# Kernel tuning notes

Hardware: AMD Instinct MI355X
Metric: run time of the kernel (lower is better)

Reference implementation:

```python
import jax, jax.numpy as jnp
import numpy as np
import math

NUM_HEADS = 16
ATTN_WIDTH = 256


def setup_inputs() -> dict:
    key = jax.random.key(0)
    ks = jax.random.split(key, 5)
    B, S, C, H = 2, 2048, 1024, 1024
    scale = 0.02
    return {
        "x": jax.random.normal(ks[0], (B, S, C), dtype=jnp.float32),
        "Wq": jax.random.normal(ks[1], (C, H), dtype=jnp.float32) * scale,
        "Wk": jax.random.normal(ks[2], (C, H), dtype=jnp.float32) * scale,
        "Wv": jax.random.normal(ks[3], (C, H), dtype=jnp.float32) * scale,
        "Wo": jax.random.normal(ks[4], (H, C), dtype=jnp.float32) * scale,
    }


def reference(x, Wq, Wk, Wv, Wo):
    B, S, C = x.shape
    H = NUM_HEADS
    dh = Wq.shape[1] // H  # head dim; Q.size(-1) in torch code

    def split_heads(t):
        # [B, S, H*dh] -> [B, H, S, dh]
        return t.reshape(B, S, H, dh).transpose(0, 2, 1, 3)

    q = split_heads(x @ Wq)
    k = split_heads(x @ Wk)
    v = split_heads(x @ Wv)

    scores = jnp.einsum("bhqd,bhkd->bhqk", q, k) / math.sqrt(dh)
    # exp-shift (first 'softmax-like' step, unnormalized)
    scores = jnp.exp(scores - jnp.max(scores, axis=-1, keepdims=True))
    # banded mask: tril(attn_width//2 - 1).triu(-(attn_width//2))
    i = jnp.arange(S)[:, None]
    j = jnp.arange(S)[None, :]
    d = j - i
    half = ATTN_WIDTH // 2
    mask = (d <= half - 1) & (d >= -half)
    scores = jnp.where(mask, scores, 0.0)
    # second softmax over the masked exp-scores (zeros contribute exp(0)=1)
    weights = jax.nn.softmax(scores, axis=-1)

    out = jnp.einsum("bhqk,bhkd->bhqd", weights, v)  # [B, H, S, dh]
    out = out.transpose(0, 2, 1, 3).reshape(B, S, H * dh)
    return out @ Wo
```

## Files before the change

kernel.cpp:

```cpp
#include <hip/hip_runtime.h>
#include <math.h>

typedef __bf16 bf16_t;
typedef bf16_t bf16x8 __attribute__((ext_vector_type(8)));
typedef bf16_t bf16x4 __attribute__((ext_vector_type(4)));
typedef float f32x4 __attribute__((ext_vector_type(4)));

constexpr int S_ = 2048;
constexpr float SCALE = 0.125f;

#define MFMA_B16(a, b, c) __builtin_amdgcn_mfma_f32_16x16x32_bf16(a, b, c, 0, 0, 0)

#define WAIT_VM0() __builtin_amdgcn_s_waitcnt(0x0F70)
#define WAIT_VM4() __builtin_amdgcn_s_waitcnt(0x0F74)
#define BARRIER()  __builtin_amdgcn_s_barrier()

typedef __attribute__((address_space(1))) const void* as1_cvp;
typedef __attribute__((address_space(3))) void* as3_vp;

__device__ __forceinline__ void gl2lds16(const void* g, void* l)
{
    __builtin_amdgcn_global_load_lds((as1_cvp)g, (as3_vp)l, 16, 0, 0);
}

#define SRC_SWZ8(lane) ((((lane) & 3) ^ (((lane) >> 3) & 3)) * 8)
#define RD_SWZ8(quad, l15) ((((quad) ^ (((l15) >> 1) & 3))) * 8)

__global__ __launch_bounds__(256) void prep(const float* __restrict__ x,
                                            const float* __restrict__ Wq,
                                            const float* __restrict__ Wk,
                                            const float* __restrict__ Wv,
                                            const float* __restrict__ Wo,
                                            bf16_t* __restrict__ xb,
                                            bf16_t* __restrict__ Wqt,
                                            bf16_t* __restrict__ Wkt,
                                            bf16_t* __restrict__ Wvt,
                                            bf16_t* __restrict__ Wot,
                                            float* __restrict__ vsp)
{
    __shared__ float T[64][65];
    const int blk = blockIdx.x;
    const int tid = threadIdx.x;
    if (blk < 1024) {
#pragma unroll
        for (int u = 0; u < 4; ++u) {
            const int g = blk * 1024 + u * 256 + tid;
            const float4 v = ((const float4*)x)[g];
            bf16x4 o;
            o[0] = (bf16_t)v.x; o[1] = (bf16_t)v.y;
            o[2] = (bf16_t)v.z; o[3] = (bf16_t)v.w;
            *(bf16x4*)&xb[(size_t)g * 4] = o;
        }
    } else if (blk < 2048) {
        const int rem = blk - 1024;
        const int wsel = rem >> 8, t = rem & 255;
        const float* src = (wsel == 0) ? Wq : (wsel == 1) ? Wk : (wsel == 2) ? Wv : Wo;
        bf16_t* dst = (wsel == 0) ? Wqt : (wsel == 1) ? Wkt : (wsel == 2) ? Wvt : Wot;
        const int k0 = (t >> 4) * 64, n0 = (t & 15) * 64;
        const int rr = tid >> 4, c4 = (tid & 15) * 4;
#pragma unroll
        for (int u = 0; u < 4; ++u) {
            const float4 v = *(const float4*)&src[(size_t)(k0 + u * 16 + rr) * 1024 + n0 + c4];
            T[u * 16 + rr][c4 + 0] = v.x; T[u * 16 + rr][c4 + 1] = v.y;
            T[u * 16 + rr][c4 + 2] = v.z; T[u * 16 + rr][c4 + 3] = v.w;
        }
        __syncthreads();
#pragma unroll
        for (int u = 0; u < 4; ++u) {
            bf16x4 o;
#pragma unroll
            for (int e = 0; e < 4; ++e) o[e] = (bf16_t)T[c4 + e][u * 16 + rr];
            *(bf16x4*)&dst[(size_t)(n0 + u * 16 + rr) * 1024 + k0 + c4] = o;
        }
    } else {
#pragma unroll
        for (int u = 0; u < 8; ++u) vsp[u * 256 + tid] = 0.f;
    }
}

template <int MODE>
__device__ __forceinline__ void mfma_gemm_body(const bf16_t* __restrict__ A,
                                               const bf16_t* __restrict__ Bt,
                                               void* __restrict__ dst,
                                               float* __restrict__ vsum_out,
                                               int m0, int n0)
{
    __shared__ bf16_t As[12288];
    __shared__ bf16_t Bs[12288];

    const int tid = threadIdx.x;
    const int lane = tid & 63, wid = tid >> 6;
    const int l15 = lane & 15, quad = lane >> 4;
    const int wm = (wid & 1) * 64, wn = (wid >> 1) * 64;

    const int srow = wid * 32 + (lane >> 2);
    const int scg8 = SRC_SWZ8(lane);
    const bf16_t* Ag0 = A  + (size_t)(m0 + srow) * 1024 + scg8;
    const bf16_t* Ag1 = A  + (size_t)(m0 + srow + 16) * 1024 + scg8;
    const bf16_t* Bg0 = Bt + (size_t)(n0 + srow) * 1024 + scg8;
    const bf16_t* Bg1 = Bt + (size_t)(n0 + srow + 16) * 1024 + scg8;

    const int rs = RD_SWZ8(quad, l15);

    f32x4 acc[4][4];
#pragma unroll
    for (int i = 0; i < 4; ++i)
#pragma unroll
        for (int j = 0; j < 4; ++j) acc[i][j] = (f32x4){0.f, 0.f, 0.f, 0.f};

#pragma unroll
    for (int p = 0; p < 2; ++p) {
        const int k0 = p * 32;
        gl2lds16(Ag0 + k0, As + p * 4096 + (wid * 2 + 0) * 512);
        gl2lds16(Ag1 + k0, As + p * 4096 + (wid * 2 + 1) * 512);
        gl2lds16(Bg0 + k0, Bs + p * 4096 + (wid * 2 + 0) * 512);
        gl2lds16(Bg1 + k0, Bs + p * 4096 + (wid * 2 + 1) * 512);
    }

#pragma unroll
    for (int it = 0; it < 32; ++it) {
        if (it < 30) WAIT_VM4(); else WAIT_VM0();
        BARRIER();
        if (it < 30) {
            const int k0 = (it + 2) * 32;
            const int sb = (it + 2) % 3;
            gl2lds16(Ag0 + k0, As + sb * 4096 + (wid * 2 + 0) * 512);
            gl2lds16(Ag1 + k0, As + sb * 4096 + (wid * 2 + 1) * 512);
            gl2lds16(Bg0 + k0, Bs + sb * 4096 + (wid * 2 + 0) * 512);
            gl2lds16(Bg1 + k0, Bs + sb * 4096 + (wid * 2 + 1) * 512);
        }
        const int cb = it % 3;
        bf16x8 af[4], bfr[4];
#pragma unroll
        for (int mt = 0; mt < 4; ++mt)
            af[mt] = *(const bf16x8*)&As[cb * 4096 + (wm + mt * 16 + l15) * 32 + rs];
#pragma unroll
        for (int nt = 0; nt < 4; ++nt)
            bfr[nt] = *(const bf16x8*)&Bs[cb * 4096 + (wn + nt * 16 + l15) * 32 + rs];
#pragma unroll
        for (int mt = 0; mt < 4; ++mt)
#pragma unroll
            for (int nt = 0; nt < 4; ++nt)
                acc[mt][nt] = MFMA_B16(bfr[nt], af[mt], acc[mt][nt]);
    }

#pragma unroll
    for (int mt = 0; mt < 4; ++mt) {
        const int m = m0 + wm + mt * 16 + l15;
#pragma unroll
        for (int nt = 0; nt < 4; ++nt) {
            const int nb = n0 + wn + nt * 16 + quad * 4;
            if (MODE == 0) {
                *(f32x4*)&((float*)dst)[(size_t)m * 1024 + nb] = acc[mt][nt];
            } else {
                const int bb = m >> 11, s = m & 2047;
                const int hh = nb >> 6, d = nb & 63;
                bf16x4 o;
#pragma unroll
                for (int u = 0; u < 4; ++u) o[u] = (bf16_t)acc[mt][nt][u];
                *(bf16x4*)&((bf16_t*)dst)[((size_t)(bb * 16 + hh) * 2048 + s) * 64 + d] = o;
            }
        }
    }

    if (MODE == 1 && vsum_out != nullptr) {
        const int bb = m0 >> 11;
#pragma unroll
        for (int nt = 0; nt < 4; ++nt) {
            f32x4 p = acc[0][nt];
#pragma unroll
            for (int mt = 1; mt < 4; ++mt) {
                p[0] += acc[mt][nt][0]; p[1] += acc[mt][nt][1];
                p[2] += acc[mt][nt][2]; p[3] += acc[mt][nt][3];
            }
#pragma unroll
            for (int st = 1; st < 16; st <<= 1) {
                p[0] += __shfl_xor(p[0], st);
                p[1] += __shfl_xor(p[1], st);
                p[2] += __shfl_xor(p[2], st);
                p[3] += __shfl_xor(p[3], st);
            }
            if (l15 == 0) {
                const int nI = n0 + wn + nt * 16 + quad * 4;
                float* vp = &vsum_out[(bb * 16 + (nI >> 6)) * 64 + (nI & 63)];
                atomicAdd(vp + 0, p[0]);
                atomicAdd(vp + 1, p[1]);
                atomicAdd(vp + 2, p[2]);
                atomicAdd(vp + 3, p[3]);
            }
        }
    }
}

__global__ __launch_bounds__(256) void gemm_qkv_mfma(const bf16_t* __restrict__ xb,
                                                     const bf16_t* __restrict__ Wqt,
                                                     const bf16_t* __restrict__ Wkt,
                                                     const bf16_t* __restrict__ Wvt,
                                                     bf16_t* Qh, bf16_t* Kh, bf16_t* Vh,
                                                     float* vsp)
{
    const bf16_t* Bt = (blockIdx.z == 0) ? Wqt : (blockIdx.z == 1) ? Wkt : Wvt;
    bf16_t* dst = (blockIdx.z == 0) ? Qh : (blockIdx.z == 1) ? Kh : Vh;
    float* vs = (blockIdx.z == 2) ? vsp : nullptr;
    mfma_gemm_body<1>(xb, Bt, dst, vs, blockIdx.y * 128, blockIdx.x * 128);
}

__global__ __launch_bounds__(256) void gemm_out_mfma(const bf16_t* __restrict__ attn,
                                                     const bf16_t* __restrict__ Wot,
                                                     float* __restrict__ out)
{
    mfma_gemm_body<0>(attn, Wot, out, nullptr, blockIdx.y * 128, blockIdx.x * 128);
}

__global__ __launch_bounds__(256) void rowmax_k(const bf16_t* __restrict__ Qh,
                                                const bf16_t* __restrict__ Kh,
                                                float* __restrict__ mrow)
{
    __shared__ bf16_t Qs[8192];
    __shared__ bf16_t Ks[8192];
    __shared__ float msh[4][8][16];

    const int tid = threadIdx.x;
    const int lane = tid & 63, wid = tid >> 6;
    const int l15 = lane & 15, quad = lane >> 4;

    const int f = blockIdx.x;
    const int seq = f >> 3;
    const int bh = (f & 7) + 8 * (seq >> 4);
    const int i0 = (seq & 15) * 128;
    const bf16_t* Qb = Qh + (size_t)bh * 131072;
    const bf16_t* Kb = Kh + (size_t)bh * 131072;

    const int ssw = SRC_SWZ8(lane);
    const int rs  = RD_SWZ8(quad, l15);

#pragma unroll
    for (int c = 0; c < 4; ++c) {
        const int g = wid * 4 + c;
        const int half = g >> 3;
        const int row = (g & 7) * 16 + (lane >> 2);
        gl2lds16(Qb + (size_t)(i0 + row) * 64 + half * 32 + ssw,
                 Qs + g * 512);
    }
    __syncthreads();

    bf16x8 af[8][2];
#pragma unroll
    for (int mt = 0; mt < 8; ++mt)
#pragma unroll
        for (int ks = 0; ks < 2; ++ks)
            af[mt][ks] = *(const bf16x8*)&Qs[ks * 4096 + (mt * 16 + l15) * 32 + rs];

    f32x4 vm[8];
#pragma unroll
    for (int mt = 0; mt < 8; ++mt)
        vm[mt] = (f32x4){-3.0e38f, -3.0e38f, -3.0e38f, -3.0e38f};

    for (int jc = 0; jc < 16; ++jc) {
        __syncthreads();
#pragma unroll
        for (int c = 0; c < 4; ++c) {
            const int g = wid * 4 + c;
            const int half = g >> 3;
            const int row = (g & 7) * 16 + (lane >> 2);
            gl2lds16(Kb + (size_t)(jc * 128 + row) * 64 + half * 32 + ssw,
                     Ks + g * 512);
        }
        __syncthreads();

#pragma unroll
        for (int ntl = 0; ntl < 2; ++ntl) {
            const int jt = wid * 2 + ntl;
            const bf16x8 b0 = *(const bf16x8*)&Ks[(jt * 16 + l15) * 32 + rs];
            const bf16x8 b1 = *(const bf16x8*)&Ks[4096 + (jt * 16 + l15) * 32 + rs];
#pragma unroll
            for (int mt = 0; mt < 8; ++mt) {
                f32x4 t = (f32x4){0.f, 0.f, 0.f, 0.f};
                t = MFMA_B16(b0, af[mt][0], t);
                t = MFMA_B16(b1, af[mt][1], t);
                vm[mt][0] = fmaxf(vm[mt][0], t[0]);
                vm[mt][1] = fmaxf(vm[mt][1], t[1]);
                vm[mt][2] = fmaxf(vm[mt][2], t[2]);
                vm[mt][3] = fmaxf(vm[mt][3], t[3]);
            }
        }
    }

#pragma unroll
    for (int mt = 0; mt < 8; ++mt) {
        float v = fmaxf(fmaxf(vm[mt][0], vm[mt][1]), fmaxf(vm[mt][2], vm[mt][3]));
        v = fmaxf(v, __shfl_xor(v, 16));
        v = fmaxf(v, __shfl_xor(v, 32));
        if (quad == 0) msh[wid][mt][l15] = v;
    }
    __syncthreads();

    if (tid < 128) {
        const int mt = tid >> 4, il = tid & 15;
        const float v = fmaxf(fmaxf(msh[0][mt][il], msh[1][mt][il]),
                              fmaxf(msh[2][mt][il], msh[3][mt][il]));
        mrow[(size_t)bh * S_ + i0 + mt * 16 + il] = v * SCALE;
    }
}

__global__ __launch_bounds__(256) void band_k(const bf16_t* __restrict__ Qh,
                                              const bf16_t* __restrict__ Kh,
                                              const bf16_t* __restrict__ Vh,
                                              const float* __restrict__ mrow,
                                              const float* __restrict__ vsp,
                                              bf16_t* __restrict__ attn)
{
    __shared__ bf16_t Qs[8192];
    __shared__ bf16_t Ks2[4096];
    __shared__ bf16_t Vt[4608];
    __shared__ bf16_t Ws[9216];
    __shared__ float zsh[4][32];

    const int tid = threadIdx.x;
    const int lane = tid & 63, wid = tid >> 6;
    const int l15 = lane & 15, quad = lane >> 4;

    const int f = blockIdx.x;
    const int seq = f >> 3;
    const int bh = (f & 7) + 8 * (seq >> 4);
    const int i0 = (seq & 15) * 128;
    const int b = bh >> 4, h = bh & 15;
    const bf16_t* Qb = Qh + (size_t)bh * 131072;
    const bf16_t* Kb = Kh + (size_t)bh * 131072;
    const bf16_t* Vb = Vh + (size_t)bh * 131072;

    const int ssw = SRC_SWZ8(lane);
    const int rs  = RD_SWZ8(quad, l15);

#pragma unroll
    for (int c = 0; c < 4; ++c) {
        const int g = wid * 4 + c;
        const int half = g >> 3;
        const int row = (g & 7) * 16 + (lane >> 2);
        gl2lds16(Qb + (size_t)(i0 + row) * 64 + half * 32 + ssw,
                 Qs + g * 512);
    }
    __syncthreads();

    bf16x8 aq[2][2];
#pragma unroll
    for (int t = 0; t < 2; ++t)
#pragma unroll
        for (int ks = 0; ks < 2; ++ks)
            aq[t][ks] = *(const bf16x8*)&Qs[ks * 4096 + ((wid * 2 + t) * 16 + l15) * 32 + rs];

    float mreg[2][4];
#pragma unroll
    for (int t = 0; t < 2; ++t)
#pragma unroll
        for (int r = 0; r < 4; ++r)
            mreg[t][r] = mrow[(size_t)bh * S_ + i0 + (wid * 2 + t) * 16 + quad * 4 + r];

    f32x4 vsd4[4];
#pragma unroll
    for (int dt = 0; dt < 4; ++dt)
        vsd4[dt] = *(const f32x4*)&vsp[bh * 64 + dt * 16 + quad * 4];

    f32x4 accO[2][4];
#pragma unroll
    for (int t = 0; t < 2; ++t)
#pragma unroll
        for (int dt = 0; dt < 4; ++dt) accO[t][dt] = (f32x4){0.f, 0.f, 0.f, 0.f};
    float zp[2][4] = {{0.f, 0.f, 0.f, 0.f}, {0.f, 0.f, 0.f, 0.f}};

    for (int cb2 = 0; cb2 < 6; ++cb2) {
        const int jb = i0 - 128 + cb2 * 64;
        if (jb < 0 || jb >= S_) continue;

        __syncthreads();
#pragma unroll
        for (int c = 0; c < 2; ++c) {
            const int g = wid * 2 + c;
            const int half = g >> 2;
            const int row = (g & 3) * 16 + (lane >> 2);
            gl2lds16(Kb + (size_t)(jb + row) * 64 + half * 32 + ssw,
                     Ks2 + g * 512);
        }
        {
            const bf16x8 v0 = *(const bf16x8*)&Vb[(size_t)(jb + lane) * 64 + wid * 16];
            const bf16x8 v1 = *(const bf16x8*)&Vb[(size_t)(jb + lane) * 64 + wid * 16 + 8];
#pragma unroll
            for (int e = 0; e < 8; ++e) {
                Vt[(wid * 16 + e) * 72 + lane] = v0[e];
                Vt[(wid * 16 + 8 + e) * 72 + lane] = v1[e];
            }
        }
        __syncthreads();

#pragma unroll
        for (int t = 0; t < 2; ++t) {
            const int mt = wid * 2 + t;
#pragma unroll
            for (int jt4 = 0; jt4 < 4; ++jt4) {
                const bf16x8 k0 = *(const bf16x8*)&Ks2[(jt4 * 16 + l15) * 32 + rs];
                const bf16x8 k1 = *(const bf16x8*)&Ks2[2048 + (jt4 * 16 + l15) * 32 + rs];
                f32x4 sc = (f32x4){0.f, 0.f, 0.f, 0.f};
                sc = MFMA_B16(aq[t][0], k0, sc);
                sc = MFMA_B16(aq[t][1], k1, sc);
#pragma unroll
                for (int r = 0; r < 4; ++r) {
                    const int ig = i0 + mt * 16 + quad * 4 + r;
                    const int jg = jb + jt4 * 16 + l15;
                    const int dd = jg - ig;
                    const bool ok = (dd >= -128) && (dd <= 127);
                    const float e1 = __expf(sc[r] * SCALE - mreg[t][r]);
                    const float wv = ok ? (__expf(e1) - 1.0f) : 0.0f;
                    const bf16_t wb = (bf16_t)wv;
                    zp[t][r] += (float)wb;
                    Ws[(mt * 16 + quad * 4 + r) * 72 + jt4 * 16 + l15] = wb;
                }
            }
        }
        __syncthreads();

#pragma unroll
        for (int ks = 0; ks < 2; ++ks) {
            bf16x8 bv[4];
#pragma unroll
            for (int dt = 0; dt < 4; ++dt)
                bv[dt] = *(const bf16x8*)&Vt[(dt * 16 + l15) * 72 + ks * 32 + quad * 8];
#pragma unroll
            for (int t = 0; t < 2; ++t) {
                const int mt = wid * 2 + t;
                const bf16x8 aw = *(const bf16x8*)&Ws[(mt * 16 + l15) * 72 + ks * 32 + quad * 8];
#pragma unroll
                for (int dt = 0; dt < 4; ++dt)
                    accO[t][dt] = MFMA_B16(bv[dt], aw, accO[t][dt]);
            }
        }
    }

#pragma unroll
    for (int t = 0; t < 2; ++t)
#pragma unroll
        for (int r = 0; r < 4; ++r) {
            float z = zp[t][r];
            z += __shfl_xor(z, 1);
            z += __shfl_xor(z, 2);
            z += __shfl_xor(z, 4);
            z += __shfl_xor(z, 8);
            if (l15 == 0) zsh[wid][t * 16 + quad * 4 + r] = z + (float)S_;
        }
    __syncthreads();

#pragma unroll
    for (int t = 0; t < 2; ++t) {
        const float rz = 1.0f / zsh[wid][t * 16 + l15];
        const int irow = i0 + (wid * 2 + t) * 16 + l15;
#pragma unroll
        for (int dt = 0; dt < 4; ++dt) {
            bf16x4 o;
#pragma unroll
            for (int r = 0; r < 4; ++r)
                o[r] = (bf16_t)((accO[t][dt][r] + vsd4[dt][r]) * rz);
            *(bf16x4*)&attn[(size_t)(b * S_ + irow) * 1024 + h * 64 + dt * 16 + quad * 4] = o;
        }
    }
}

extern "C" void kernel_launch(void* const* d_in, const int* in_sizes, int n_in,
                              void* d_out, int out_size, void* d_ws, size_t ws_size,
                              hipStream_t stream)
{
    const float* x  = (const float*)d_in[0];
    const float* Wq = (const float*)d_in[1];
    const float* Wk = (const float*)d_in[2];
    const float* Wv = (const float*)d_in[3];
    const float* Wo = (const float*)d_in[4];
    float* out = (float*)d_out;

    char* ws = (char*)d_ws;
    bf16_t* xb   = (bf16_t*)(ws + 0);
    bf16_t* Wqt  = (bf16_t*)(ws + 8388608);
    bf16_t* Wkt  = (bf16_t*)(ws + 10485760);
    bf16_t* Wvt  = (bf16_t*)(ws + 12582912);
    bf16_t* Wot  = (bf16_t*)(ws + 14680064);
    bf16_t* Qh   = (bf16_t*)(ws + 16777216);
    bf16_t* Kh   = (bf16_t*)(ws + 25165824);
    bf16_t* Vh   = (bf16_t*)(ws + 33554432);
    bf16_t* attn = (bf16_t*)(ws + 41943040);
    float*  vsp  = (float*)(ws + 50331648);
    float*  mrow = (float*)(ws + 50339840);

    prep<<<2049, 256, 0, stream>>>(x, Wq, Wk, Wv, Wo, xb, Wqt, Wkt, Wvt, Wot, vsp);
    gemm_qkv_mfma<<<dim3(8, 32, 3), 256, 0, stream>>>(xb, Wqt, Wkt, Wvt, Qh, Kh, Vh, vsp);
    rowmax_k<<<512, 256, 0, stream>>>(Qh, Kh, mrow);
    band_k<<<512, 256, 0, stream>>>(Qh, Kh, Vh, mrow, vsp, attn);
    gemm_out_mfma<<<dim3(8, 32), 256, 0, stream>>>(attn, Wot, out);
}
```

Before: 187.2 us.

## Enlarge QKV GEMM tiles to 256x256 and triple-buffer K loads in rowmax

The QKV projection GEMM becomes a dedicated 512-thread kernel with 256x256 output tiles, each wave holding 8x4 accumulators. This raises operand reuse per LDS load but cuts the grid from 768 to 192 blocks, which may underfill the CUs and raises register pressure. The rowmax kernel replaces its sync-load-sync loop over K chunks with a three-buffer async prefetch pipeline, overlapping global-to-LDS copies with the MFMA work.

```diff
diff --git a/kernel.cpp b/kernel.cpp
--- a/kernel.cpp
+++ b/kernel.cpp
@@ -78,12 +78,126 @@
     }
 }
 
-template <int MODE>
-__device__ __forceinline__ void mfma_gemm_body(const bf16_t* __restrict__ A,
-                                               const bf16_t* __restrict__ Bt,
-                                               void* __restrict__ dst,
-                                               float* __restrict__ vsum_out,
-                                               int m0, int n0)
+__global__ __launch_bounds__(512, 2) void gemm_qkv_mfma(const bf16_t* __restrict__ xb,
+                                                        const bf16_t* __restrict__ Wqt,
+                                                        const bf16_t* __restrict__ Wkt,
+                                                        const bf16_t* __restrict__ Wvt,
+                                                        bf16_t* Qh, bf16_t* Kh, bf16_t* Vh,
+                                                        float* vsp)
+{
+    __shared__ bf16_t As[24576];
+    __shared__ bf16_t Bs[24576];
+
+    const bf16_t* A  = xb;
+    const bf16_t* Bt = (blockIdx.z == 0) ? Wqt : (blockIdx.z == 1) ? Wkt : Wvt;
+    bf16_t* dst = (blockIdx.z == 0) ? Qh : (blockIdx.z == 1) ? Kh : Vh;
+    const bool dovs = (blockIdx.z == 2);
+
+    const int tid = threadIdx.x;
+    const int lane = tid & 63, wid = tid >> 6;
+    const int l15 = lane & 15, quad = lane >> 4;
+    const int wm = (wid & 1) * 128, wn = (wid >> 1) * 64;
+    const int m0 = blockIdx.y * 256, n0 = blockIdx.x * 256;
+
+    const int srow = wid * 32 + (lane >> 2);
+    const int scg8 = SRC_SWZ8(lane);
+    const bf16_t* Ag0 = A  + (size_t)(m0 + srow) * 1024 + scg8;
+    const bf16_t* Ag1 = A  + (size_t)(m0 + srow + 16) * 1024 + scg8;
+    const bf16_t* Bg0 = Bt + (size_t)(n0 + srow) * 1024 + scg8;
+    const bf16_t* Bg1 = Bt + (size_t)(n0 + srow + 16) * 1024 + scg8;
+
+    const int rs = RD_SWZ8(quad, l15);
+
+    f32x4 acc[8][4];
+#pragma unroll
+    for (int i = 0; i < 8; ++i)
+#pragma unroll
+        for (int j = 0; j < 4; ++j) acc[i][j] = (f32x4){0.f, 0.f, 0.f, 0.f};
+
+#pragma unroll
+    for (int p = 0; p < 2; ++p) {
+        const int k0 = p * 32;
+        gl2lds16(Ag0 + k0, As + p * 8192 + (wid * 2 + 0) * 512);
+        gl2lds16(Ag1 + k0, As + p * 8192 + (wid * 2 + 1) * 512);
+        gl2lds16(Bg0 + k0, Bs + p * 8192 + (wid * 2 + 0) * 512);
+        gl2lds16(Bg1 + k0, Bs + p * 8192 + (wid * 2 + 1) * 512);
+    }
+
+#pragma unroll
+    for (int it = 0; it < 32; ++it) {
+        if (it < 30) WAIT_VM4(); else WAIT_VM0();
+        BARRIER();
+        if (it < 30) {
+            const int k0 = (it + 2) * 32;
+            const int sb = (it + 2) % 3;
+            gl2lds16(Ag0 + k0, As + sb * 8192 + (wid * 2 + 0) * 512);
+            gl2lds16(Ag1 + k0, As + sb * 8192 + (wid * 2 + 1) * 512);
+            gl2lds16(Bg0 + k0, Bs + sb * 8192 + (wid * 2 + 0) * 512);
+            gl2lds16(Bg1 + k0, Bs + sb * 8192 + (wid * 2 + 1) * 512);
+        }
+        const int cb = it % 3;
+        bf16x8 af[8], bfr[4];
+#pragma unroll
+        for (int mt = 0; mt < 8; ++mt)
+            af[mt] = *(const bf16x8*)&As[cb * 8192 + (wm + mt * 16 + l15) * 32 + rs];
+#pragma unroll
+        for (int nt = 0; nt < 4; ++nt)
+            bfr[nt] = *(const bf16x8*)&Bs[cb * 8192 + (wn + nt * 16 + l15) * 32 + rs];
+#pragma unroll
+        for (int mt = 0; mt < 8; ++mt)
+#pragma unroll
+            for (int nt = 0; nt < 4; ++nt)
+                acc[mt][nt] = MFMA_B16(bfr[nt], af[mt], acc[mt][nt]);
+    }
+
+    const int bb = m0 >> 11;
+#pragma unroll
+    for (int mt = 0; mt < 8; ++mt) {
+        const int m = m0 + wm + mt * 16 + l15;
+        const int s = m & 2047;
+#pragma unroll
+        for (int nt = 0; nt < 4; ++nt) {
+            const int nb = n0 + wn + nt * 16 + quad * 4;
+            const int hh = nb >> 6, d = nb & 63;
+            bf16x4 o;
+#pragma unroll
+            for (int u = 0; u < 4; ++u) o[u] = (bf16_t)acc[mt][nt][u];
+            *(bf16x4*)&dst[((size_t)(bb * 16 + hh) * 2048 + s) * 64 + d] = o;
+        }
+    }
+
+    if (dovs) {
+#pragma unroll
+        for (int nt = 0; nt < 4; ++nt) {
+            f32x4 p = acc[0][nt];
+#pragma unroll
+            for (int mt = 1; mt < 8; ++mt) {
+                p[0] += acc[mt][nt][0]; p[1] += acc[mt][nt][1];
+                p[2] += acc[mt][nt][2]; p[3] += acc[mt][nt][3];
+            }
+#pragma unroll
+            for (int st = 1; st < 16; st <<= 1) {
+                p[0] += __shfl_xor(p[0], st);
+                p[1] += __shfl_xor(p[1], st);
+                p[2] += __shfl_xor(p[2], st);
+                p[3] += __shfl_xor(p[3], st);
+            }
+            if (l15 == 0) {
+                const int nI = n0 + wn + nt * 16 + quad * 4;
+                float* vp = &vsp[(bb * 16 + (nI >> 6)) * 64 + (nI & 63)];
+                atomicAdd(vp + 0, p[0]);
+                atomicAdd(vp + 1, p[1]);
+                atomicAdd(vp + 2, p[2]);
+                atomicAdd(vp + 3, p[3]);
+            }
+        }
+    }
+}
+
+__device__ __forceinline__ void mfma_gemm128(const bf16_t* __restrict__ A,
+                                             const bf16_t* __restrict__ Bt,
+                                             float* __restrict__ dst,
+                                             int m0, int n0)
 {
     __shared__ bf16_t As[12288];
     __shared__ bf16_t Bs[12288];
@@ -150,66 +264,16 @@
 #pragma unroll
         for (int nt = 0; nt < 4; ++nt) {
             const int nb = n0 + wn + nt * 16 + quad * 4;
-            if (MODE == 0) {
-                *(f32x4*)&((float*)dst)[(size_t)m * 1024 + nb] = acc[mt][nt];
-            } else {
-                const int bb = m >> 11, s = m & 2047;
-                const int hh = nb >> 6, d = nb & 63;
-                bf16x4 o;
-#pragma unroll
-                for (int u = 0; u < 4; ++u) o[u] = (bf16_t)acc[mt][nt][u];
-                *(bf16x4*)&((bf16_t*)dst)[((size_t)(bb * 16 + hh) * 2048 + s) * 64 + d] = o;
-            }
-        }
-    }
-
-    if (MODE == 1 && vsum_out != nullptr) {
-        const int bb = m0 >> 11;
-#pragma unroll
-        for (int nt = 0; nt < 4; ++nt) {
-            f32x4 p = acc[0][nt];
-#pragma unroll
-            for (int mt = 1; mt < 4; ++mt) {
-                p[0] += acc[mt][nt][0]; p[1] += acc[mt][nt][1];
-                p[2] += acc[mt][nt][2]; p[3] += acc[mt][nt][3];
-            }
-#pragma unroll
-            for (int st = 1; st < 16; st <<= 1) {
-                p[0] += __shfl_xor(p[0], st);
-                p[1] += __shfl_xor(p[1], st);
-                p[2] += __shfl_xor(p[2], st);
-                p[3] += __shfl_xor(p[3], st);
-            }
-            if (l15 == 0) {
-                const int nI = n0 + wn + nt * 16 + quad * 4;
-                float* vp = &vsum_out[(bb * 16 + (nI >> 6)) * 64 + (nI & 63)];
-                atomicAdd(vp + 0, p[0]);
-                atomicAdd(vp + 1, p[1]);
-                atomicAdd(vp + 2, p[2]);
-                atomicAdd(vp + 3, p[3]);
-            }
-        }
-    }
-}
-
-__global__ __launch_bounds__(256) void gemm_qkv_mfma(const bf16_t* __restrict__ xb,
-                                                     const bf16_t* __restrict__ Wqt,
-                                                     const bf16_t* __restrict__ Wkt,
-                                                     const bf16_t* __restrict__ Wvt,
-                                                     bf16_t* Qh, bf16_t* Kh, bf16_t* Vh,
-                                                     float* vsp)
-{
-    const bf16_t* Bt = (blockIdx.z == 0) ? Wqt : (blockIdx.z == 1) ? Wkt : Wvt;
-    bf16_t* dst = (blockIdx.z == 0) ? Qh : (blockIdx.z == 1) ? Kh : Vh;
-    float* vs = (blockIdx.z == 2) ? vsp : nullptr;
-    mfma_gemm_body<1>(xb, Bt, dst, vs, blockIdx.y * 128, blockIdx.x * 128);
+            *(f32x4*)&dst[(size_t)m * 1024 + nb] = acc[mt][nt];
+        }
+    }
 }
 
 __global__ __launch_bounds__(256) void gemm_out_mfma(const bf16_t* __restrict__ attn,
                                                      const bf16_t* __restrict__ Wot,
                                                      float* __restrict__ out)
 {
-    mfma_gemm_body<0>(attn, Wot, out, nullptr, blockIdx.y * 128, blockIdx.x * 128);
+    mfma_gemm128(attn, Wot, out, blockIdx.y * 128, blockIdx.x * 128);
 }
 
 __global__ __launch_bounds__(256) void rowmax_k(const bf16_t* __restrict__ Qh,
@@ -217,7 +281,7 @@
                                                 float* __restrict__ mrow)
 {
     __shared__ bf16_t Qs[8192];
-    __shared__ bf16_t Ks[8192];
+    __shared__ bf16_t Ks[24576];
     __shared__ float msh[4][8][16];
 
     const int tid = threadIdx.x;
@@ -242,37 +306,53 @@
         gl2lds16(Qb + (size_t)(i0 + row) * 64 + half * 32 + ssw,
                  Qs + g * 512);
     }
-    __syncthreads();
-
-    bf16x8 af[8][2];
-#pragma unroll
-    for (int mt = 0; mt < 8; ++mt)
-#pragma unroll
-        for (int ks = 0; ks < 2; ++ks)
-            af[mt][ks] = *(const bf16x8*)&Qs[ks * 4096 + (mt * 16 + l15) * 32 + rs];
-
-    f32x4 vm[8];
-#pragma unroll
-    for (int mt = 0; mt < 8; ++mt)
-        vm[mt] = (f32x4){-3.0e38f, -3.0e38f, -3.0e38f, -3.0e38f};
-
-    for (int jc = 0; jc < 16; ++jc) {
-        __syncthreads();
+#pragma unroll
+    for (int p = 0; p < 2; ++p)
 #pragma unroll
         for (int c = 0; c < 4; ++c) {
             const int g = wid * 4 + c;
             const int half = g >> 3;
             const int row = (g & 7) * 16 + (lane >> 2);
-            gl2lds16(Kb + (size_t)(jc * 128 + row) * 64 + half * 32 + ssw,
-                     Ks + g * 512);
-        }
-        __syncthreads();
-
+            gl2lds16(Kb + (size_t)(p * 128 + row) * 64 + half * 32 + ssw,
+                     Ks + p * 8192 + g * 512);
+        }
+    __syncthreads();
+
+    bf16x8 af[8][2];
+#pragma unroll
+    for (int mt = 0; mt < 8; ++mt)
+#pragma unroll
+        for (int ks = 0; ks < 2; ++ks)
+            af[mt][ks] = *(const bf16x8*)&Qs[ks * 4096 + (mt * 16 + l15) * 32 + rs];
+
+    f32x4 vm[8];
+#pragma unroll
+    for (int mt = 0; mt < 8; ++mt)
+        vm[mt] = (f32x4){-3.0e38f, -3.0e38f, -3.0e38f, -3.0e38f};
+
+#pragma unroll
+    for (int jc = 0; jc < 16; ++jc) {
+        if (jc >= 2) {
+            if (jc < 15) WAIT_VM4(); else WAIT_VM0();
+        }
+        __builtin_amdgcn_s_barrier();
+        if (jc < 14) {
+            const int sb = (jc + 2) % 3;
+#pragma unroll
+            for (int c = 0; c < 4; ++c) {
+                const int g = wid * 4 + c;
+                const int half = g >> 3;
+                const int row = (g & 7) * 16 + (lane >> 2);
+                gl2lds16(Kb + (size_t)((jc + 2) * 128 + row) * 64 + half * 32 + ssw,
+                         Ks + sb * 8192 + g * 512);
+            }
+        }
+        const int cbuf = jc % 3;
 #pragma unroll
         for (int ntl = 0; ntl < 2; ++ntl) {
             const int jt = wid * 2 + ntl;
-            const bf16x8 b0 = *(const bf16x8*)&Ks[(jt * 16 + l15) * 32 + rs];
-            const bf16x8 b1 = *(const bf16x8*)&Ks[4096 + (jt * 16 + l15) * 32 + rs];
+            const bf16x8 b0 = *(const bf16x8*)&Ks[cbuf * 8192 + (jt * 16 + l15) * 32 + rs];
+            const bf16x8 b1 = *(const bf16x8*)&Ks[cbuf * 8192 + 4096 + (jt * 16 + l15) * 32 + rs];
 #pragma unroll
             for (int mt = 0; mt < 8; ++mt) {
                 f32x4 t = (f32x4){0.f, 0.f, 0.f, 0.f};
@@ -488,7 +568,7 @@
     float*  mrow = (float*)(ws + 50339840);
 
     prep<<<2049, 256, 0, stream>>>(x, Wq, Wk, Wv, Wo, xb, Wqt, Wkt, Wvt, Wot, vsp);
-    gemm_qkv_mfma<<<dim3(8, 32, 3), 256, 0, stream>>>(xb, Wqt, Wkt, Wvt, Qh, Kh, Vh, vsp);
+    gemm_qkv_mfma<<<dim3(4, 16, 3), 512, 0, stream>>>(xb, Wqt, Wkt, Wvt, Qh, Kh, Vh, vsp);
     rowmax_k<<<512, 256, 0, stream>>>(Qh, Kh, mrow);
     band_k<<<512, 256, 0, stream>>>(Qh, Kh, Vh, mrow, vsp, attn);
     gemm_out_mfma<<<dim3(8, 32), 256, 0, stream>>>(attn, Wot, out);
```

Measured after the change: 254.3 us. +35.8%, slower.

## Double-buffer K tiles in rowmax kernel to overlap loads with MFMA

Applied to the files above, without the earlier changes.

The rowmax kernel now keeps two K tiles in LDS. It prefetches the next 128-row chunk while computing on the current one, using partial vmcnt waits and raw barriers in place of two full syncthreads per iteration. The goal is to hide global-to-LDS latency behind the QK^T MFMA work. In exchange, K shared memory doubles, which may lower occupancy, and correctness now depends on the waitcnt values matching the number of loads in flight.

```diff
diff --git a/kernel.cpp b/kernel.cpp
--- a/kernel.cpp
+++ b/kernel.cpp
@@ -217,7 +217,7 @@
                                                 float* __restrict__ mrow)
 {
     __shared__ bf16_t Qs[8192];
-    __shared__ bf16_t Ks[8192];
+    __shared__ bf16_t Ks[16384];
     __shared__ float msh[4][8][16];
 
     const int tid = threadIdx.x;
@@ -234,13 +234,22 @@
     const int ssw = SRC_SWZ8(lane);
     const int rs  = RD_SWZ8(quad, l15);
 
+    const int g    = wid * 4;
+    const int srow = (lane >> 2);
+
 #pragma unroll
     for (int c = 0; c < 4; ++c) {
-        const int g = wid * 4 + c;
-        const int half = g >> 3;
-        const int row = (g & 7) * 16 + (lane >> 2);
-        gl2lds16(Qb + (size_t)(i0 + row) * 64 + half * 32 + ssw,
-                 Qs + g * 512);
+        const int gg = g + c;
+        const int half = gg >> 3;
+        const int row = (gg & 7) * 16 + srow;
+        gl2lds16(Qb + (size_t)(i0 + row) * 64 + half * 32 + ssw, Qs + gg * 512);
+    }
+#pragma unroll
+    for (int c = 0; c < 4; ++c) {
+        const int gg = g + c;
+        const int half = gg >> 3;
+        const int row = (gg & 7) * 16 + srow;
+        gl2lds16(Kb + (size_t)row * 64 + half * 32 + ssw, Ks + gg * 512);
     }
     __syncthreads();
 
@@ -256,23 +265,31 @@
     for (int mt = 0; mt < 8; ++mt)
         vm[mt] = (f32x4){-3.0e38f, -3.0e38f, -3.0e38f, -3.0e38f};
 
+#pragma unroll 2
     for (int jc = 0; jc < 16; ++jc) {
-        __syncthreads();
-#pragma unroll
-        for (int c = 0; c < 4; ++c) {
-            const int g = wid * 4 + c;
-            const int half = g >> 3;
-            const int row = (g & 7) * 16 + (lane >> 2);
-            gl2lds16(Kb + (size_t)(jc * 128 + row) * 64 + half * 32 + ssw,
-                     Ks + g * 512);
-        }
-        __syncthreads();
-
+        BARRIER();
+        if (jc < 15) {
+            const int sb = (jc + 1) & 1;
+#pragma unroll
+            for (int c = 0; c < 4; ++c) {
+                const int gg = g + c;
+                const int half = gg >> 3;
+                const int row = (gg & 7) * 16 + srow;
+                gl2lds16(Kb + (size_t)((jc + 1) * 128 + row) * 64 + half * 32 + ssw,
+                         Ks + sb * 8192 + gg * 512);
+            }
+            WAIT_VM4();
+        } else {
+            WAIT_VM0();
+        }
+        BARRIER();
+
+        const int cbuf = jc & 1;
 #pragma unroll
         for (int ntl = 0; ntl < 2; ++ntl) {
             const int jt = wid * 2 + ntl;
-            const bf16x8 b0 = *(const bf16x8*)&Ks[(jt * 16 + l15) * 32 + rs];
-            const bf16x8 b1 = *(const bf16x8*)&Ks[4096 + (jt * 16 + l15) * 32 + rs];
+            const bf16x8 b0 = *(const bf16x8*)&Ks[cbuf * 8192 + (jt * 16 + l15) * 32 + rs];
+            const bf16x8 b1 = *(const bf16x8*)&Ks[cbuf * 8192 + 4096 + (jt * 16 + l15) * 32 + rs];
 #pragma unroll
             for (int mt = 0; mt < 8; ++mt) {
                 f32x4 t = (f32x4){0.f, 0.f, 0.f, 0.f};
```

Result: no change. 189.0 us (+1.0%).
